# Performance work log

Measured on AMD Instinct MI355X. Metric: run time of the kernel, lower is better.

## Reference

```python
import jax, jax.numpy as jnp
import numpy as np

EMBED_DIM = 1024
NUM_HEADS = 16
HEAD_DIM = EMBED_DIM // NUM_HEADS
SEG_LENS = [1024, 2048, 4096]
DIL_RATIOS = [1, 2, 4]
NEG = -1e8  # lse fill value used by sparse_to_dense


def setup_inputs() -> dict:
    root = jax.random.key(0)
    ks = jax.random.split(root, 12)
    B, L, E = 1, 4096, EMBED_DIM
    s = 0.02
    return {
        "query": jax.random.normal(ks[0], (B, L, E), jnp.float32),
        "key": jax.random.normal(ks[1], (B, L, E), jnp.float32),
        "value": jax.random.normal(ks[2], (B, L, E), jnp.float32),
        "Wq": jax.random.normal(ks[3], (E, E), jnp.float32) * s,
        "bq": jnp.zeros((E,), jnp.float32),
        "Wk": jax.random.normal(ks[4], (E, E), jnp.float32) * s,
        "bk": jnp.zeros((E,), jnp.float32),
        "Wv": jax.random.normal(ks[5], (E, E), jnp.float32) * s,
        "bv": jnp.zeros((E,), jnp.float32),
        "Wo": jax.random.normal(ks[6], (E, E), jnp.float32) * s,
        "bo": jnp.zeros((E,), jnp.float32),
    }


def _branch(q, k, v, sl, dr, L):
    """One (segment_length, dilated_ratio) branch.
    q,k,v: (B, L, H, D). Returns dense out (B, H, L, D) and lse (B, H, L).
    """
    B = q.shape[0]
    H, D = NUM_HEADS, HEAD_DIM
    sl = min(sl, L)
    pad = (-L) % sl
    if pad:
        pw = ((0, 0), (0, pad), (0, 0), (0, 0))
        q, k, v = jnp.pad(q, pw), jnp.pad(k, pw), jnp.pad(v, pw)
    n = (L + pad) // sl  # segments
    qs = q.reshape(B * n, sl, H, D)
    ks = k.reshape(B * n, sl, H, D)
    vs = v.reshape(B * n, sl, H, D)
    # dense_to_sparse: head j (group r = j // (H//dr)) keeps positions i*dr + r
    hg = H // dr
    g = sl // dr
    grp = jnp.arange(H) // hg                      # (H,)
    pos = jnp.arange(g)[:, None] * dr + grp[None]  # (g, H) dense positions
    hidx = jnp.arange(H)[None, :]
    sp = lambda x: x[:, pos, hidx, :]              # (B*n, g, H, D)
    qd, kd, vd = sp(qs), sp(ks), sp(vs)
    # causal attention within each sparse segment (flash_attn semantics)
    scores = jnp.einsum('bqhd,bkhd->bhqk', qd, kd) * (D ** -0.5)
    mask = jnp.tril(jnp.ones((g, g), bool))
    scores = jnp.where(mask, scores, -jnp.inf)
    lse = jax.nn.logsumexp(scores, axis=-1)        # (B*n, H, g)
    o = jnp.einsum('bhqk,bkhd->bqhd', jnp.exp(scores - lse[..., None]), vd)
    # sparse_to_dense: scatter back onto dense positions, NEG elsewhere
    hcol = jnp.arange(H)[:, None]                  # (H,1)
    od = jnp.zeros((B * n, H, sl, D), o.dtype).at[:, hcol, pos.T].set(
        o.transpose(0, 2, 1, 3))
    ld = jnp.zeros((B * n, H, sl), lse.dtype).at[:, hcol, pos.T].set(lse)
    ld = jnp.where(ld == 0.0, NEG, ld)  # matches masked_fill_(lse == 0, -1e8)
    od = od.reshape(B, n, H, sl, D).transpose(0, 2, 1, 3, 4)
    od = od.reshape(B, H, n * sl, D)[:, :, :L]
    ld = ld.reshape(B, n, H, sl).transpose(0, 2, 1, 3).reshape(B, H, n * sl)[:, :, :L]
    return od, ld


def reference(query, key, value, Wq, bq, Wk, bk, Wv, bv, Wo, bo):
    B, L, E = query.shape
    H, D = NUM_HEADS, HEAD_DIM
    q = (query @ Wq.T + bq).reshape(B, L, H, D)
    k = (key @ Wk.T + bk).reshape(B, L, H, D)
    v = (value @ Wv.T + bv).reshape(B, L, H, D)
    outs, lses = [], []
    for sl, dr in zip(SEG_LENS, DIL_RATIOS):
        o, l = _branch(q, k, v, sl, dr, L)
        outs.append(o)
        lses.append(l)
    lse_all = jnp.stack(lses, 0)[..., None]        # (nb, B, H, L, 1)
    m = lse_all.max(0)
    w = jnp.exp(lse_all - m)
    w = w / w.sum(0)                               # softmax merge weights
    w = jax.lax.stop_gradient(w)                   # torch computes under no_grad
    out = sum(o * wi.astype(o.dtype) for o, wi in zip(outs, w))  # (B,H,L,D)
    out = out.transpose(0, 2, 1, 3).reshape(B, L, E)
    return out @ Wo.T + bo
```

## Files before the change

### kernel.cpp

```cpp
#include <hip/hip_runtime.h>
#include <math.h>


#define L_SEQ 4096
#define EDIM  1024
#define NH    16
#define HD    64
#define GLEN  1024

typedef __bf16 bf16;
typedef __bf16 bf16x8 __attribute__((ext_vector_type(8)));
typedef __bf16 bf16x4 __attribute__((ext_vector_type(4)));
typedef short  s16x4  __attribute__((ext_vector_type(4)));
typedef float  f32x4  __attribute__((ext_vector_type(4)));

template <bool B> struct Flag { static constexpr bool v = B; };

__device__ __forceinline__ void gload16(const bf16* g, bf16* l) {
  __builtin_amdgcn_global_load_lds(
      (__attribute__((address_space(1))) void*)(const_cast<bf16*>(g)),
      (__attribute__((address_space(3))) void*)(l),
      16, 0, 0);
}

__device__ __forceinline__ f32x4 mfma16x16x16_bf16(bf16x4 a, bf16x4 b, f32x4 c) {
#if defined(__HIP_DEVICE_COMPILE__)
  union { bf16x4 h; s16x4 s; } ua, ub;
  ua.h = a; ub.h = b;
  return __builtin_amdgcn_mfma_f32_16x16x16bf16_1k(ua.s, ub.s, c, 0, 0, 0);
#else
  (void)a; (void)b;
  return c;
#endif
}

__device__ __forceinline__ float fast_exp2(float x) {
#if __has_builtin(__builtin_amdgcn_exp2f)
  return __builtin_amdgcn_exp2f(x);
#else
  return __expf(x * 0.6931471805599453f);
#endif
}

__global__ __launch_bounds__(256) void cvt_kernel(
    const float* q, const float* k, const float* v,
    const float* wq, const float* wk, const float* wv, const float* wo,
    bf16* oq, bf16* ok, bf16* ov,
    bf16* owq, bf16* owk, bf16* owv, bf16* owo)
{
  const float* src; bf16* dst; int n;
  switch (blockIdx.y) {
    case 0: src = q;  dst = oq;  n = L_SEQ*EDIM; break;
    case 1: src = k;  dst = ok;  n = L_SEQ*EDIM; break;
    case 2: src = v;  dst = ov;  n = L_SEQ*EDIM; break;
    case 3: src = wq; dst = owq; n = EDIM*EDIM; break;
    case 4: src = wk; dst = owk; n = EDIM*EDIM; break;
    case 5: src = wv; dst = owv; n = EDIM*EDIM; break;
    default: src = wo; dst = owo; n = EDIM*EDIM; break;
  }
  int i = (blockIdx.x * 256 + threadIdx.x) * 8;
  if (i >= n) return;
  const float4* s4 = (const float4*)(src + i);
  float4 a = s4[0], b = s4[1];
  bf16x8 o = { (bf16)a.x, (bf16)a.y, (bf16)a.z, (bf16)a.w,
               (bf16)b.x, (bf16)b.y, (bf16)b.z, (bf16)b.w };
  *(bf16x8*)(dst + i) = o;
}

template <typename OutT>
__device__ __forceinline__ void gemm_body(const bf16* __restrict__ A,
                                          const bf16* __restrict__ W,
                                          const float* __restrict__ bias,
                                          OutT* __restrict__ C)
{
  constexpr int K = 1024;
  __shared__ __align__(16) bf16 lA[2][128 * 32];
  __shared__ __align__(16) bf16 lB[2][128 * 32];

  const int tid  = threadIdx.x;
  const int lane = tid & 63;
  const int w    = tid >> 6;
  const int quad = lane >> 4;
  const int l16  = lane & 15;
  const int wr   = w >> 1, wc = w & 1;
  const int ly = blockIdx.x * 4 + (blockIdx.y >> 3);
  const int lx = blockIdx.y & 7;
  const int row0 = ly * 128;
  const int col0 = lx * 128;

  f32x4 acc[4][4] = {};

  const int c0 = tid, c1 = tid + 256;
  const bf16* Ab0 = A + (size_t)(row0 + (c0 >> 2)) * K + (c0 & 3) * 8;
  const bf16* Ab1 = A + (size_t)(row0 + (c1 >> 2)) * K + (c1 & 3) * 8;
  const bf16* Bb0 = W + (size_t)(col0 + (c0 >> 2)) * K + (c0 & 3) * 8;
  const bf16* Bb1 = W + (size_t)(col0 + (c1 >> 2)) * K + (c1 & 3) * 8;

  auto stage = [&](int kt, int buf) {
    gload16(Ab0 + kt, &lA[buf][c0 * 8]);
    gload16(Ab1 + kt, &lA[buf][c1 * 8]);
    gload16(Bb0 + kt, &lB[buf][c0 * 8]);
    gload16(Bb1 + kt, &lB[buf][c1 * 8]);
  };

  stage(0, 0);
  __syncthreads();

  for (int t = 0; t < 32; ++t) {
    const int cur = t & 1;
    if (t < 31) stage((t + 1) * 32, cur ^ 1);

    bf16x8 af[4], bfrag[4];
#pragma unroll
    for (int mi = 0; mi < 4; mi++)
      af[mi] = *(const bf16x8*)&lA[cur][(wr * 64 + mi * 16 + l16) * 32 + quad * 8];
#pragma unroll
    for (int ni = 0; ni < 4; ni++)
      bfrag[ni] = *(const bf16x8*)&lB[cur][(wc * 64 + ni * 16 + l16) * 32 + quad * 8];
#pragma unroll
    for (int mi = 0; mi < 4; mi++)
#pragma unroll
      for (int ni = 0; ni < 4; ni++)
        acc[mi][ni] = __builtin_amdgcn_mfma_f32_16x16x32_bf16(
            af[mi], bfrag[ni], acc[mi][ni], 0, 0, 0);

    __syncthreads();
  }

#pragma unroll
  for (int mi = 0; mi < 4; mi++) {
#pragma unroll
    for (int ni = 0; ni < 4; ni++) {
      const int gcol = col0 + wc * 64 + ni * 16 + l16;
      const float bv = bias[gcol];
#pragma unroll
      for (int r = 0; r < 4; r++) {
        const int grow = row0 + wr * 64 + mi * 16 + quad * 4 + r;
        C[(size_t)grow * 1024 + gcol] = (OutT)(acc[mi][ni][r] + bv);
      }
    }
  }
}

__global__ __launch_bounds__(256) void gemm_qkv_kernel(
    const bf16* xq, const bf16* xk, const bf16* xv,
    const bf16* wq, const bf16* wk, const bf16* wv,
    const float* bq, const float* bk, const float* bv,
    bf16* q, bf16* k, bf16* v)
{
  const bf16 *A, *W; const float* bias; bf16* C;
  if (blockIdx.z == 0)      { A = xq; W = wq; bias = bq; C = q; }
  else if (blockIdx.z == 1) { A = xk; W = wk; bias = bk; C = k; }
  else                      { A = xv; W = wv; bias = bv; C = v; }
  gemm_body<bf16>(A, W, bias, C);
}

__global__ __launch_bounds__(256) void gemm_out_kernel(
    const bf16* A, const bf16* W, const float* bias, float* C)
{
  gemm_body<float>(A, W, bias, C);
}

__global__ __launch_bounds__(256) void vtrans_kernel(
    const bf16* __restrict__ v, bf16* vt0, bf16* vt1, bf16* vt2)
{
  __shared__ __align__(16) bf16 ltile[64 * 72];
  const int bid = blockIdx.x;
  int sl, dr, rem, shift; bf16* vt;
  if (bid < 1024)      { sl = 1024; dr = 1; rem = bid;        vt = vt0; shift = 4; }
  else if (bid < 1536) { sl = 2048; dr = 2; rem = bid - 1024; vt = vt1; shift = 3; }
  else                 { sl = 4096; dr = 4; rem = bid - 1536; vt = vt2; shift = 2; }
  const int ktile = rem & 15;
  const int h     = (rem >> 4) & 15;
  const int seg   = rem >> 8;
  const int grp   = h >> shift;
  const int segbase = seg * sl;
  const int tid = threadIdx.x;
  {
    const int i = tid >> 2, dc = tid & 3;
    const size_t p = (size_t)(segbase + (ktile * 64 + i) * dr + grp);
    const bf16* src = v + p * EDIM + h * 64 + dc * 16;
    *(uint4*)&ltile[i * 72 + dc * 16]     = *(const uint4*)(src);
    *(uint4*)&ltile[i * 72 + dc * 16 + 8] = *(const uint4*)(src + 8);
  }
  __syncthreads();
  {
    const int d = tid >> 2, kc = tid & 3;
    __align__(16) bf16 tmp[16];
#pragma unroll
    for (int j = 0; j < 16; j++) tmp[j] = ltile[(kc * 16 + j) * 72 + d];
    const int p2 = kc >> 1, half = kc & 1;
    bf16* dst = vt + ((size_t)(seg * NH + h) * 64 + d) * GLEN + ktile * 64
                   + p2 * 32 + half * 4;
#pragma unroll
    for (int q = 0; q < 4; q++) {
      bf16x4 piece = { tmp[q * 4 + 0], tmp[q * 4 + 1],
                       tmp[q * 4 + 2], tmp[q * 4 + 3] };
      *(bf16x4*)(dst + q * 8) = piece;
    }
  }
}

__global__ __launch_bounds__(256, 4) void attn_kernel(
    const bf16* __restrict__ qg, const bf16* __restrict__ kg,
    const bf16* vt0, const bf16* vt1, const bf16* vt2,
    bf16* o0, bf16* o1, bf16* o2,
    float* l0, float* l1, float* l2)
{
  __shared__ __align__(16) bf16 lK[2][64 * 64];
  __shared__ __align__(16) bf16 lV[2][64 * 64];

  const int bid0 = blockIdx.x;
  const int o = (bid0 & 7) * 112 + (bid0 >> 3);

  int sl, dr, rem, shift;
  const bf16* vt; bf16* ob; float* lseb;
  if (o < 512)      { sl = 1024; dr = 1; rem = o;       vt = vt0; ob = o0; lseb = l0; shift = 4; }
  else if (o < 768) { sl = 2048; dr = 2; rem = o - 512; vt = vt1; ob = o1; lseb = l1; shift = 3; }
  else              { sl = 4096; dr = 4; rem = o - 768; vt = vt2; ob = o2; lseb = l2; shift = 2; }
  const int j   = rem & 7;
  const int h   = (rem >> 3) & 15;
  const int seg = rem >> 7;
  const int qtA = 15 - j;
  const int qtB = j;
  const int grp = h >> shift;
  const int segbase = seg * sl;

  const int tid = threadIdx.x, lane = tid & 63, w = tid >> 6;
  const int quad = lane >> 4, l16 = lane & 15;
  const int rs8 = l16 & 7;

  auto loadq = [&](int qt, bf16x8& a0, bf16x8& a1) {
    const int qi = qt * 64 + w * 16 + l16;
    const size_t p = (size_t)(segbase + qi * dr + grp);
    const bf16* qp = qg + p * EDIM + h * 64 + quad * 8;
    a0 = *(const bf16x8*)(qp);
    a1 = *(const bf16x8*)(qp + 32);
  };
  bf16x8 qaA0, qaA1, qaB0, qaB1;
  loadq(qtA, qaA0, qaA1);
  loadq(qtB, qaB0, qaB1);

  f32x4 OA[4] = {}, OB[4] = {};
  f32x4 lsA = {0.f, 0.f, 0.f, 0.f};
  f32x4 lsB = {0.f, 0.f, 0.f, 0.f};
  float mA = -__builtin_inff();
  float mB = -__builtin_inff();
  const bf16x4 ONES = { (bf16)1.f, (bf16)1.f, (bf16)1.f, (bf16)1.f };

  const bf16* vbase = vt + (size_t)(seg * NH + h) * 64 * GLEN;
  const int c0 = tid, c1 = tid + 256;
  const int r0 = c0 >> 3, sw0 = ((c0 & 7) ^ (r0 & 7));
  const int r1 = c1 >> 3, sw1 = ((c1 & 7) ^ (r1 & 7));

  const bf16* kp0 = kg + (size_t)(segbase + r0 * dr + grp) * EDIM + h * 64 + sw0 * 8;
  const bf16* kp1 = kg + (size_t)(segbase + r1 * dr + grp) * EDIM + h * 64 + sw1 * 8;
  const bf16* vp0 = vbase + (size_t)r0 * GLEN + sw0 * 8;
  const bf16* vp1 = vbase + (size_t)r1 * GLEN + sw1 * 8;
  const size_t kstep = (size_t)64 * dr * EDIM;

  auto stage = [&](int buf) {
    gload16(kp0, &lK[buf][c0 * 8]);
    gload16(kp1, &lK[buf][c1 * 8]);
    gload16(vp0, &lV[buf][c0 * 8]);
    gload16(vp1, &lV[buf][c1 * 8]);
    kp0 += kstep; kp1 += kstep; vp0 += 64; vp1 += 64;
  };

  const float CS = 0.18033688011112042f;
  const float NEGINF = -__builtin_inff();
  const int qiA = qtA * 64 + w * 16 + l16;
  const int qiB = qtB * 64 + w * 16 + l16;

  const int kb0 = l16 * 64 + ((quad ^ rs8) * 8);
  const int kb1 = l16 * 64 + (((4 + quad) ^ rs8) * 8);
  const int vb0 = l16 * 64;

  auto comp = [&](auto hasB_, auto diagA_, auto diagB_, int kt) {
    constexpr bool HAS_B  = decltype(hasB_)::v;
    constexpr bool DIAG_A = decltype(diagA_)::v;
    constexpr bool DIAG_B = decltype(diagB_)::v;
    const bf16* bK = lK[kt & 1];
    const bf16* bV = lV[kt & 1];

    f32x4 sA[4], sB[4];
#pragma unroll
    for (int t = 0; t < 4; t++) {
      const bool aA = !DIAG_A || t <= w;
      const bool aB = HAS_B && (!DIAG_B || t <= w);
      if (aA || aB) {
        bf16x8 ka0 = *(const bf16x8*)&bK[kb0 + t * 1024];
        bf16x8 ka1 = *(const bf16x8*)&bK[kb1 + t * 1024];
        if (aA) {
          sA[t] = f32x4{0.f, 0.f, 0.f, 0.f};
          sA[t] = __builtin_amdgcn_mfma_f32_16x16x32_bf16(ka0, qaA0, sA[t], 0, 0, 0);
          sA[t] = __builtin_amdgcn_mfma_f32_16x16x32_bf16(ka1, qaA1, sA[t], 0, 0, 0);
        }
        if (aB) {
          sB[t] = f32x4{0.f, 0.f, 0.f, 0.f};
          sB[t] = __builtin_amdgcn_mfma_f32_16x16x32_bf16(ka0, qaB0, sB[t], 0, 0, 0);
          sB[t] = __builtin_amdgcn_mfma_f32_16x16x32_bf16(ka1, qaB1, sB[t], 0, 0, 0);
        }
      }
    }

    f32x4 mvA = {NEGINF, NEGINF, NEGINF, NEGINF};
    f32x4 mvB = {NEGINF, NEGINF, NEGINF, NEGINF};
#pragma unroll
    for (int t = 0; t < 4; t++) {
      if (!DIAG_A || t <= w) {
#pragma unroll
        for (int r = 0; r < 4; r++) {
          float sv = sA[t][r];
          if (DIAG_A) {
            const int kj = kt * 64 + t * 16 + quad * 4 + r;
            if (kj > qiA) sv = NEGINF;
          }
          sA[t][r] = sv;
          mvA[r] = fmaxf(mvA[r], sv);
        }
      }
      if (HAS_B && (!DIAG_B || t <= w)) {
#pragma unroll
        for (int r = 0; r < 4; r++) {
          float sv = sB[t][r];
          if (DIAG_B) {
            const int kj = kt * 64 + t * 16 + quad * 4 + r;
            if (kj > qiB) sv = NEGINF;
          }
          sB[t][r] = sv;
          mvB[r] = fmaxf(mvB[r], sv);
        }
      }
    }
    float mrA = fmaxf(fmaxf(mvA[0], mvA[1]), fmaxf(mvA[2], mvA[3]));
    float mrB = fmaxf(fmaxf(mvB[0], mvB[1]), fmaxf(mvB[2], mvB[3]));
    mrA = fmaxf(mrA, __shfl_xor(mrA, 16, 64));
    mrA = fmaxf(mrA, __shfl_xor(mrA, 32, 64));
    if constexpr (HAS_B) {
      mrB = fmaxf(mrB, __shfl_xor(mrB, 16, 64));
      mrB = fmaxf(mrB, __shfl_xor(mrB, 32, 64));
    }

    {
      const float mnew = fmaxf(mA, mrA * CS);
      if (!__all(mnew - mA <= 8.0f)) {
        const float alpha = fast_exp2(mA - mnew);
#pragma unroll
        for (int nf = 0; nf < 4; nf++)
#pragma unroll
          for (int r = 0; r < 4; r++) OA[nf][r] *= alpha;
#pragma unroll
        for (int r = 0; r < 4; r++) lsA[r] *= alpha;
        mA = mnew;
      }
    }
    if constexpr (HAS_B) {
      const float mnew = fmaxf(mB, mrB * CS);
      if (!__all(mnew - mB <= 8.0f)) {
        const float alpha = fast_exp2(mB - mnew);
#pragma unroll
        for (int nf = 0; nf < 4; nf++)
#pragma unroll
          for (int r = 0; r < 4; r++) OB[nf][r] *= alpha;
#pragma unroll
        for (int r = 0; r < 4; r++) lsB[r] *= alpha;
        mB = mnew;
      }
    }

    bf16x4 pbA[4], pbB[4];
#pragma unroll
    for (int t = 0; t < 4; t++) {
      if (!DIAG_A || t <= w) {
#pragma unroll
        for (int r = 0; r < 4; r++)
          pbA[t][r] = (bf16)fast_exp2(__builtin_fmaf(sA[t][r], CS, -mA));
      }
      if (HAS_B && (!DIAG_B || t <= w)) {
#pragma unroll
        for (int r = 0; r < 4; r++)
          pbB[t][r] = (bf16)fast_exp2(__builtin_fmaf(sB[t][r], CS, -mB));
      }
    }

#pragma unroll
    for (int p2 = 0; p2 < 2; p2++) {
      const int t0 = 2 * p2, t1 = t0 + 1;
      const bool aA0 = !DIAG_A || t0 <= w;
      const bool aA1 = !DIAG_A || t1 <= w;
      const bool aB0 = HAS_B && (!DIAG_B || t0 <= w);
      const bool aB1 = HAS_B && (!DIAG_B || t1 <= w);
      if (aA0 || aA1 || aB0 || aB1) {
        const int cx = ((p2 * 4 + quad) ^ rs8) * 8;
#pragma unroll
        for (int nf = 0; nf < 4; nf++) {
          bf16x8 va8 = *(const bf16x8*)&bV[vb0 + nf * 1024 + cx];
          bf16x4 vlo = __builtin_shufflevector(va8, va8, 0, 1, 2, 3);
          bf16x4 vhi = __builtin_shufflevector(va8, va8, 4, 5, 6, 7);
          if (aA0) OA[nf] = mfma16x16x16_bf16(vlo, pbA[t0], OA[nf]);
          if (aA1) OA[nf] = mfma16x16x16_bf16(vhi, pbA[t1], OA[nf]);
          if (aB0) OB[nf] = mfma16x16x16_bf16(vlo, pbB[t0], OB[nf]);
          if (aB1) OB[nf] = mfma16x16x16_bf16(vhi, pbB[t1], OB[nf]);
        }
        if (aA0) lsA = mfma16x16x16_bf16(ONES, pbA[t0], lsA);
        if (aA1) lsA = mfma16x16x16_bf16(ONES, pbA[t1], lsA);
        if (aB0) lsB = mfma16x16x16_bf16(ONES, pbB[t0], lsB);
        if (aB1) lsB = mfma16x16x16_bf16(ONES, pbB[t1], lsB);
      }
    }
  };

  stage(0);
  int kt = 0;
  for (; kt < qtB; kt++) {
    __syncthreads();
    stage((kt + 1) & 1);
    comp(Flag<true>{}, Flag<false>{}, Flag<false>{}, kt);
  }
  __syncthreads();
  stage((kt + 1) & 1);
  comp(Flag<true>{}, Flag<false>{}, Flag<true>{}, kt);
  kt++;
  for (; kt < qtA; kt++) {
    __syncthreads();
    stage((kt + 1) & 1);
    comp(Flag<false>{}, Flag<false>{}, Flag<false>{}, kt);
  }
  __syncthreads();
  comp(Flag<false>{}, Flag<true>{}, Flag<false>{}, kt);

  auto epilogue = [&](const f32x4 (&Oa)[4], float m_r, float l_r, int qt) {
    const int qi = qt * 64 + w * 16 + l16;
    const float linv = 1.0f / l_r;
    const int pdense = segbase + qi * dr + grp;
    bf16* orow = ob + (size_t)pdense * EDIM + h * 64;
#pragma unroll
    for (int nf = 0; nf < 4; nf++) {
      bf16x4 ov;
#pragma unroll
      for (int r = 0; r < 4; r++) ov[r] = (bf16)(Oa[nf][r] * linv);
      *(bf16x4*)(orow + nf * 16 + quad * 4) = ov;
    }
    if (quad == 0)
      lseb[h * L_SEQ + pdense] = m_r * 0.6931471805599453f + __logf(l_r);
  };
  epilogue(OA, mA, lsA[0], qtA);
  epilogue(OB, mB, lsB[0], qtB);
}

__global__ __launch_bounds__(256) void merge_kernel(
    const bf16* __restrict__ o0, const bf16* __restrict__ o1, const bf16* __restrict__ o2,
    const float* __restrict__ l0, const float* __restrict__ l1, const float* __restrict__ l2,
    bf16* __restrict__ merged)
{
  const int idx = blockIdx.x * 256 + threadIdx.x;
  const int dc = idx & 7;
  const int h  = (idx >> 3) & 15;
  const int p  = idx >> 7;
  const bool c1 = ((p & 1) == (h >> 3));
  const bool c2 = ((p & 3) == (h >> 2));
  const float s0 = l0[h * L_SEQ + p];
  const float s1 = c1 ? l1[h * L_SEQ + p] : -__builtin_inff();
  const float s2 = c2 ? l2[h * L_SEQ + p] : -__builtin_inff();
  const float mx = fmaxf(s0, fmaxf(s1, s2));
  float w0 = __expf(s0 - mx);
  float w1 = c1 ? __expf(s1 - mx) : 0.f;
  float w2 = c2 ? __expf(s2 - mx) : 0.f;
  const float inv = 1.0f / (w0 + w1 + w2);
  w0 *= inv; w1 *= inv; w2 *= inv;

  const size_t off = (size_t)p * EDIM + h * 64 + dc * 8;
  float acc[8];
  bf16x8 a0 = *(const bf16x8*)(o0 + off);
#pragma unroll
  for (int j = 0; j < 8; j++) acc[j] = w0 * (float)a0[j];
  if (c1) {
    bf16x8 a1 = *(const bf16x8*)(o1 + off);
#pragma unroll
    for (int j = 0; j < 8; j++) acc[j] += w1 * (float)a1[j];
  }
  if (c2) {
    bf16x8 a2 = *(const bf16x8*)(o2 + off);
#pragma unroll
    for (int j = 0; j < 8; j++) acc[j] += w2 * (float)a2[j];
  }
  bf16x8 r;
#pragma unroll
  for (int j = 0; j < 8; j++) r[j] = (bf16)acc[j];
  *(bf16x8*)(merged + off) = r;
}

extern "C" void kernel_launch(void* const* d_in, const int* in_sizes, int n_in,
                              void* d_out, int out_size, void* d_ws, size_t ws_size,
                              hipStream_t stream)
{
  (void)in_sizes; (void)n_in; (void)out_size; (void)ws_size;
  const float* query = (const float*)d_in[0];
  const float* key   = (const float*)d_in[1];
  const float* value = (const float*)d_in[2];
  const float* Wq = (const float*)d_in[3];
  const float* bq = (const float*)d_in[4];
  const float* Wk = (const float*)d_in[5];
  const float* bk = (const float*)d_in[6];
  const float* Wv = (const float*)d_in[7];
  const float* bv = (const float*)d_in[8];
  const float* Wo = (const float*)d_in[9];
  const float* bo = (const float*)d_in[10];

  char* base = (char*)d_ws;
  size_t off = 0;
  auto take = [&](size_t nbytes) -> char* {
    char* p = base + off;
    off += (nbytes + 255) & ~(size_t)255;
    return p;
  };
  const size_t LE2 = (size_t)L_SEQ * EDIM * 2;
  const size_t EE2 = (size_t)EDIM * EDIM * 2;
  bf16* xq  = (bf16*)take(LE2);
  bf16* xk  = (bf16*)take(LE2);
  bf16* xv  = (bf16*)take(LE2);
  bf16* wqb = (bf16*)take(EE2);
  bf16* wkb = (bf16*)take(EE2);
  bf16* wvb = (bf16*)take(EE2);
  bf16* wob = (bf16*)take(EE2);
  bf16* qb  = (bf16*)take(LE2);
  bf16* kb  = (bf16*)take(LE2);
  bf16* vb  = (bf16*)take(LE2);
  bf16* vt0 = (bf16*)take((size_t)4 * NH * HD * GLEN * 2);
  bf16* vt1 = (bf16*)take((size_t)2 * NH * HD * GLEN * 2);
  bf16* vt2 = (bf16*)take((size_t)1 * NH * HD * GLEN * 2);
  float* lse0 = (float*)take((size_t)NH * L_SEQ * 4);
  float* lse1 = (float*)take((size_t)NH * L_SEQ * 4);
  float* lse2 = (float*)take((size_t)NH * L_SEQ * 4);
  bf16* merged = (bf16*)take(LE2);
  bf16* o0 = xq; bf16* o1 = xk; bf16* o2 = xv;

  dim3 blk(256);
  cvt_kernel<<<dim3(2048, 7), blk, 0, stream>>>(
      query, key, value, Wq, Wk, Wv, Wo, xq, xk, xv, wqb, wkb, wvb, wob);
  gemm_qkv_kernel<<<dim3(8, 32, 3), blk, 0, stream>>>(
      xq, xk, xv, wqb, wkb, wvb, bq, bk, bv, qb, kb, vb);
  vtrans_kernel<<<dim3(1792), blk, 0, stream>>>(vb, vt0, vt1, vt2);
  attn_kernel<<<dim3(896), blk, 0, stream>>>(
      qb, kb, vt0, vt1, vt2, o0, o1, o2, lse0, lse1, lse2);
  merge_kernel<<<dim3(2048), blk, 0, stream>>>(
      o0, o1, o2, lse0, lse1, lse2, merged);
  gemm_out_kernel<<<dim3(8, 32), blk, 0, stream>>>(merged, wob, bo, (float*)d_out);
}
```

Baseline: 228.8 us.

## Triple-buffer GEMM LDS staging with vmcnt waits and flatten convert grid

The GEMM main loop moves from double to triple buffering in LDS. Loads are issued two tiles ahead, and a partial s_waitcnt vmcnt plus a raw s_barrier replaces the full __syncthreads, so global loads overlap compute better. Separately, the fp32-to-bf16 convert kernel now uses a flat 1D grid with no idle blocks: the old 2048x7 grid left most weight-row blocks exiting early. The cost is 50% more LDS per GEMM block, which may lower occupancy, and correctness now depends on the hand-written vmcnt counts.

```diff
diff --git a/kernel.cpp b/kernel.cpp
--- a/kernel.cpp
+++ b/kernel.cpp
@@ -48,23 +48,25 @@
     bf16* oq, bf16* ok, bf16* ov,
     bf16* owq, bf16* owk, bf16* owv, bf16* owo)
 {
-  const float* src; bf16* dst; int n;
-  switch (blockIdx.y) {
-    case 0: src = q;  dst = oq;  n = L_SEQ*EDIM; break;
-    case 1: src = k;  dst = ok;  n = L_SEQ*EDIM; break;
-    case 2: src = v;  dst = ov;  n = L_SEQ*EDIM; break;
-    case 3: src = wq; dst = owq; n = EDIM*EDIM; break;
-    case 4: src = wk; dst = owk; n = EDIM*EDIM; break;
-    case 5: src = wv; dst = owv; n = EDIM*EDIM; break;
-    default: src = wo; dst = owo; n = EDIM*EDIM; break;
-  }
-  int i = (blockIdx.x * 256 + threadIdx.x) * 8;
-  if (i >= n) return;
-  const float4* s4 = (const float4*)(src + i);
+  const size_t e = ((size_t)blockIdx.x * 256 + threadIdx.x) * 8;
+  const float* src; bf16* dst; size_t off;
+  if (e < (size_t)12 * 1024 * 1024) {
+    const int s = (int)(e >> 22);
+    off = e & (((size_t)1 << 22) - 1);
+    src = (s == 0) ? q : (s == 1) ? k : v;
+    dst = (s == 0) ? oq : (s == 1) ? ok : ov;
+  } else {
+    const size_t e2 = e - (size_t)12 * 1024 * 1024;
+    const int s = (int)(e2 >> 20);
+    off = e2 & (((size_t)1 << 20) - 1);
+    src = (s == 0) ? wq : (s == 1) ? wk : (s == 2) ? wv : wo;
+    dst = (s == 0) ? owq : (s == 1) ? owk : (s == 2) ? owv : owo;
+  }
+  const float4* s4 = (const float4*)(src + off);
   float4 a = s4[0], b = s4[1];
   bf16x8 o = { (bf16)a.x, (bf16)a.y, (bf16)a.z, (bf16)a.w,
                (bf16)b.x, (bf16)b.y, (bf16)b.z, (bf16)b.w };
-  *(bf16x8*)(dst + i) = o;
+  *(bf16x8*)(dst + off) = o;
 }
 
 template <typename OutT>
@@ -74,8 +76,8 @@
                                           OutT* __restrict__ C)
 {
   constexpr int K = 1024;
-  __shared__ __align__(16) bf16 lA[2][128 * 32];
-  __shared__ __align__(16) bf16 lB[2][128 * 32];
+  __shared__ __align__(16) bf16 lA[3][128 * 32];
+  __shared__ __align__(16) bf16 lB[3][128 * 32];
 
   const int tid  = threadIdx.x;
   const int lane = tid & 63;
@@ -103,13 +105,7 @@
     gload16(Bb1 + kt, &lB[buf][c1 * 8]);
   };
 
-  stage(0, 0);
-  __syncthreads();
-
-  for (int t = 0; t < 32; ++t) {
-    const int cur = t & 1;
-    if (t < 31) stage((t + 1) * 32, cur ^ 1);
-
+  auto comptile = [&](int cur) {
     bf16x8 af[4], bfrag[4];
 #pragma unroll
     for (int mi = 0; mi < 4; mi++)
@@ -123,9 +119,27 @@
       for (int ni = 0; ni < 4; ni++)
         acc[mi][ni] = __builtin_amdgcn_mfma_f32_16x16x32_bf16(
             af[mi], bfrag[ni], acc[mi][ni], 0, 0, 0);
-
-    __syncthreads();
-  }
+  };
+
+  stage(0, 0);
+  stage(32, 1);
+  asm volatile("s_waitcnt vmcnt(4)" ::: "memory");
+  __builtin_amdgcn_s_barrier();
+  asm volatile("" ::: "memory");
+
+#pragma unroll 3
+  for (int t = 0; t < 30; ++t) {
+    stage((t + 2) * 32, (t + 2) % 3);
+    comptile(t % 3);
+    asm volatile("s_waitcnt vmcnt(4)" ::: "memory");
+    __builtin_amdgcn_s_barrier();
+    asm volatile("" ::: "memory");
+  }
+  comptile(0);
+  asm volatile("s_waitcnt vmcnt(0)" ::: "memory");
+  __builtin_amdgcn_s_barrier();
+  asm volatile("" ::: "memory");
+  comptile(1);
 
 #pragma unroll
   for (int mi = 0; mi < 4; mi++) {
@@ -537,7 +551,7 @@
   bf16* o0 = xq; bf16* o1 = xk; bf16* o2 = xv;
 
   dim3 blk(256);
-  cvt_kernel<<<dim3(2048, 7), blk, 0, stream>>>(
+  cvt_kernel<<<dim3(8192), blk, 0, stream>>>(
       query, key, value, Wq, Wk, Wv, Wo, xq, xk, xv, wqb, wkb, wvb, wob);
   gemm_qkv_kernel<<<dim3(8, 32, 3), blk, 0, stream>>>(
       xq, xk, xv, wqb, wkb, wvb, bq, bk, bv, qb, kb, vb);
```

Result: no change. 227.6 us (-0.5%).
